# Kernel tuning notes

Hardware: AMD Instinct MI355X
Metric: run time of the kernel (lower is better)

## Reference

```python
import jax, jax.numpy as jnp
import numpy as np

B, L, D_MODEL = 2, 2048, 768
H, F = 12, 16            # num_heads, feature_dim
DH = D_MODEL // H        # head_dim = 64


def setup_inputs() -> dict:
    key = jax.random.key(0)
    ks = jax.random.split(key, 5)
    scale = lambda fan_in: 1.0 / np.sqrt(fan_in)
    return {
        "hidden_states": jax.random.normal(ks[0], (B, L, D_MODEL), jnp.float32),
        "Wq": jax.random.normal(ks[1], (D_MODEL, H * F), jnp.float32) * scale(D_MODEL),
        "Wk": jax.random.normal(ks[2], (D_MODEL, H * F), jnp.float32) * scale(D_MODEL),
        "Wv": jax.random.normal(ks[3], (D_MODEL, H * DH), jnp.float32) * scale(D_MODEL),
        "Wo": jax.random.normal(ks[4], (H * DH, D_MODEL), jnp.float32) * scale(H * DH),
    }


def reference(hidden_states, Wq, Wk, Wv, Wo):
    b, l, d = hidden_states.shape
    dt = hidden_states.dtype
    # projections -> (b, h, l, feat)
    q = (hidden_states @ Wq).reshape(b, l, H, F).transpose(0, 2, 1, 3)
    k = (hidden_states @ Wk).reshape(b, l, H, F).transpose(0, 2, 1, 3)
    v = (hidden_states @ Wv).reshape(b, l, H, DH).transpose(0, 2, 1, 3)

    n = jnp.arange(1, l + 1, dtype=dt)[:, None]          # (l, 1)
    mean_keys = jnp.cumsum(k, axis=2) / n                # running mean over seq
    center_keys = k - mean_keys
    mean_values = jnp.cumsum(v, axis=2) / n
    center_values = v - mean_values

    qK = jnp.einsum('bhqi,bhpi->bhqp', q, center_keys)   # (b,h,l,l)
    causal = jnp.tril(jnp.ones((l, l), dtype=bool))
    qK = jnp.where(causal, qK, jnp.zeros((), dt))

    inv_2d = 1.0 / (2.0 * DH)
    # cumsum over query dim, then sum over key dim (faithful to original)
    qK_squared = jnp.sum(jnp.cumsum(qK * qK * inv_2d, axis=2), axis=3)  # (b,h,l)
    denominator = n[:, 0] + qK_squared                   # (b,h,l) via broadcast

    qKV = jnp.einsum('bhqp,bhpi->bhqi', qK, center_values) / jnp.sqrt(jnp.asarray(DH, dt))
    y = mean_values + qKV / denominator[..., None]       # (b,h,l,dh)
    y = y.transpose(0, 2, 1, 3).reshape(b, l, H * DH)
    return y @ Wo
```

## Files before the change

kernel.cpp:

```cpp
#include <hip/hip_runtime.h>
#include <hip/hip_bf16.h>
#include <stdint.h>

constexpr int B_ = 2, L_ = 2048, DM = 768, NH_ = 12, F_ = 16, DH_ = 64;
constexpr int CH = 32, NCH = L_ / CH;

typedef __bf16 bf16x8 __attribute__((ext_vector_type(8)));
typedef __bf16 bf16x4 __attribute__((ext_vector_type(4)));
typedef float f32x4 __attribute__((ext_vector_type(4)));
typedef float f32x16 __attribute__((ext_vector_type(16)));
typedef unsigned u32x2 __attribute__((ext_vector_type(2)));

#define GLOAD16(g, l)                                                        \
  __builtin_amdgcn_global_load_lds(                                          \
      (const __attribute__((address_space(1))) void*)(g),                    \
      (__attribute__((address_space(3))) void*)(l), 16, 0, 0)

__device__ __forceinline__ unsigned cvt_pk_bf16(float lo, float hi) {
  unsigned r;
  asm("v_cvt_pk_bf16_f32 %0, %1, %2" : "=v"(r) : "v"(lo), "v"(hi));
  return r;
}

union pa_u { unsigned u[4]; bf16x8 v; };

__device__ __forceinline__ void pack_p(const f32x16& s, pa_u& pa0, pa_u& pa1) {
  unsigned w0 = cvt_pk_bf16(s[0], s[1]),   w1 = cvt_pk_bf16(s[2], s[3]);
  unsigned w2 = cvt_pk_bf16(s[4], s[5]),   w3 = cvt_pk_bf16(s[6], s[7]);
  unsigned w4 = cvt_pk_bf16(s[8], s[9]),   w5 = cvt_pk_bf16(s[10], s[11]);
  unsigned w6 = cvt_pk_bf16(s[12], s[13]), w7 = cvt_pk_bf16(s[14], s[15]);
  u32x2 r0 = __builtin_amdgcn_permlane32_swap(w0, w2, false, false);
  u32x2 r1 = __builtin_amdgcn_permlane32_swap(w1, w3, false, false);
  u32x2 r2 = __builtin_amdgcn_permlane32_swap(w4, w6, false, false);
  u32x2 r3 = __builtin_amdgcn_permlane32_swap(w5, w7, false, false);
  pa0.u[0] = r0[0]; pa0.u[1] = r1[0]; pa0.u[2] = r0[1]; pa0.u[3] = r1[1];
  pa1.u[0] = r2[0]; pa1.u[1] = r3[0]; pa1.u[2] = r2[1]; pa1.u[3] = r3[1];
}

__global__ __launch_bounds__(256)
void prep_kernel(const float* __restrict__ hs, const float* __restrict__ Wq,
                 const float* __restrict__ Wk, const float* __restrict__ Wv,
                 const float* __restrict__ Wo, __bf16* __restrict__ hsb,
                 __bf16* __restrict__ WqkvT, __bf16* __restrict__ WoT) {
  int bx = blockIdx.x;
  if (bx < 1440) {
    const float* src; __bf16* dst; int C, kt, nt;
    int id = bx;
    if (id < 144)      { src = Wq; dst = WqkvT;             C = 192; kt = id / 6;  nt = id % 6;  }
    else if (id < 288) { id -= 144; src = Wk; dst = WqkvT + (size_t)192 * 768; C = 192; kt = id / 6;  nt = id % 6;  }
    else if (id < 864) { id -= 288; src = Wv; dst = WqkvT + (size_t)384 * 768; C = 768; kt = id / 24; nt = id % 24; }
    else               { id -= 864; src = Wo; dst = WoT;    C = 768; kt = id / 24; nt = id % 24; }
    __shared__ float ld[32][33];
    int tid = threadIdx.x;
    int r = tid >> 3, cg = tid & 7;
    int k0 = kt * 32, n0 = nt * 32;
    float4 v = *(const float4*)(src + (size_t)(k0 + r) * C + n0 + cg * 4);
    ld[r][cg * 4 + 0] = v.x;
    ld[r][cg * 4 + 1] = v.y;
    ld[r][cg * 4 + 2] = v.z;
    ld[r][cg * 4 + 3] = v.w;
    __syncthreads();
    int nl = tid >> 3, kg = tid & 7;
    bf16x4 o;
#pragma unroll
    for (int j = 0; j < 4; j++) o[j] = (__bf16)ld[kg * 4 + j][nl];
    *(bf16x4*)(dst + (size_t)(n0 + nl) * 768 + k0 + kg * 4) = o;
  } else {
    int base = (bx - 1440) * 2048 + threadIdx.x * 8;
    float4 a = *(const float4*)(hs + base);
    float4 b4 = *(const float4*)(hs + base + 4);
    bf16x8 o;
    o[0] = (__bf16)a.x;  o[1] = (__bf16)a.y;  o[2] = (__bf16)a.z;  o[3] = (__bf16)a.w;
    o[4] = (__bf16)b4.x; o[5] = (__bf16)b4.y; o[6] = (__bf16)b4.z; o[7] = (__bf16)b4.w;
    *(bf16x8*)(hsb + base) = o;
  }
}

template<int BN>
__global__ __launch_bounds__(256)
void gemm_bf16(const __bf16* __restrict__ A, const __bf16* __restrict__ Bt,
               int M, int N, int K, float* __restrict__ C) {
  __shared__ __align__(16) __bf16 Al[2][128 * 32];
  __shared__ __align__(16) __bf16 Bl[2][BN * 32];
  int tid = threadIdx.x;
  int m0 = blockIdx.y * 128, n0 = blockIdx.x * BN;
  int w = tid >> 6, l = tid & 63, lr = l & 15, lg = l >> 4;
  constexpr int MI = (BN == 128) ? 4 : 2;
  int rowb = (BN == 128) ? (w >> 1) * 64 : w * 32;
  int colb = (BN == 128) ? (w & 1) * 64 : 0;
  f32x4 acc[MI][4] = {};
  const __bf16* Ab = A + (size_t)m0 * K;
  const __bf16* Bb = Bt + (size_t)n0 * K;
  int nt = K / 32;

  auto stage = [&](int buf, int k0) {
#pragma unroll
    for (int i = 0; i < 2; i++) {
      int idx = i * 256 + tid;
      GLOAD16(Ab + (size_t)(idx >> 2) * K + k0 + (idx & 3) * 8, &Al[buf][idx * 8]);
    }
    if constexpr (BN == 128) {
#pragma unroll
      for (int i = 0; i < 2; i++) {
        int idx = i * 256 + tid;
        GLOAD16(Bb + (size_t)(idx >> 2) * K + k0 + (idx & 3) * 8, &Bl[buf][idx * 8]);
      }
    } else {
      GLOAD16(Bb + (size_t)(tid >> 2) * K + k0 + (tid & 3) * 8, &Bl[buf][tid * 8]);
    }
  };

  stage(0, 0);
  asm volatile("s_waitcnt vmcnt(0)" ::: "memory");
  __syncthreads();
  int cur = 0;
  for (int t = 0; t < nt; t++) {
    if (t + 1 < nt) stage(cur ^ 1, (t + 1) * 32);
    bf16x8 af[MI], bfr[4];
#pragma unroll
    for (int mi = 0; mi < MI; mi++)
      af[mi] = *(const bf16x8*)&Al[cur][(rowb + mi * 16 + lr) * 32 + lg * 8];
#pragma unroll
    for (int ni = 0; ni < 4; ni++)
      bfr[ni] = *(const bf16x8*)&Bl[cur][(colb + ni * 16 + lr) * 32 + lg * 8];
#pragma unroll
    for (int mi = 0; mi < MI; mi++)
#pragma unroll
      for (int ni = 0; ni < 4; ni++)
        acc[mi][ni] = __builtin_amdgcn_mfma_f32_16x16x32_bf16(
            af[mi], bfr[ni], acc[mi][ni], 0, 0, 0);
    asm volatile("s_waitcnt vmcnt(0)" ::: "memory");
    __syncthreads();
    cur ^= 1;
  }

#pragma unroll
  for (int mi = 0; mi < MI; mi++)
#pragma unroll
    for (int ni = 0; ni < 4; ni++) {
      int n = n0 + colb + ni * 16 + lr;
#pragma unroll
      for (int r = 0; r < 4; r++) {
        int m = m0 + rowb + mi * 16 + lg * 4 + r;
        C[(size_t)m * N + n] = acc[mi][ni][r];
      }
    }
}

__global__ __launch_bounds__(256)
void gemm_proj(const __bf16* __restrict__ A, const __bf16* __restrict__ Bt,
               int K, __bf16* __restrict__ Qh, __bf16* __restrict__ Kh,
               __bf16* __restrict__ Vh, float* __restrict__ csum) {
  __shared__ __align__(16) __bf16 Al[2][128 * 32];
  __shared__ __align__(16) __bf16 Bl[2][64 * 32];
  __shared__ float csl[4][64];
  int tid = threadIdx.x;
  int m0 = blockIdx.y * 128, n0 = blockIdx.x * 64;
  int w = tid >> 6, l = tid & 63, lr = l & 15, lg = l >> 4;
  int rowb = w * 32;
  f32x4 acc[2][4] = {};
  const __bf16* Ab = A + (size_t)m0 * K;
  const __bf16* Bb = Bt + (size_t)n0 * K;
  int nt = K / 32;
  auto stage = [&](int buf, int k0) {
#pragma unroll
    for (int i = 0; i < 2; i++) {
      int idx = i * 256 + tid;
      GLOAD16(Ab + (size_t)(idx >> 2) * K + k0 + (idx & 3) * 8, &Al[buf][idx * 8]);
    }
    GLOAD16(Bb + (size_t)(tid >> 2) * K + k0 + (tid & 3) * 8, &Bl[buf][tid * 8]);
  };
  stage(0, 0);
  asm volatile("s_waitcnt vmcnt(0)" ::: "memory");
  __syncthreads();
  int cur = 0;
  for (int t = 0; t < nt; t++) {
    if (t + 1 < nt) stage(cur ^ 1, (t + 1) * 32);
    bf16x8 af[2], bfr[4];
#pragma unroll
    for (int mi = 0; mi < 2; mi++)
      af[mi] = *(const bf16x8*)&Al[cur][(rowb + mi * 16 + lr) * 32 + lg * 8];
#pragma unroll
    for (int ni = 0; ni < 4; ni++)
      bfr[ni] = *(const bf16x8*)&Bl[cur][(ni * 16 + lr) * 32 + lg * 8];
#pragma unroll
    for (int mi = 0; mi < 2; mi++)
#pragma unroll
      for (int ni = 0; ni < 4; ni++)
        acc[mi][ni] = __builtin_amdgcn_mfma_f32_16x16x32_bf16(
            af[mi], bfr[ni], acc[mi][ni], 0, 0, 0);
    asm volatile("s_waitcnt vmcnt(0)" ::: "memory");
    __syncthreads();
    cur ^= 1;
  }
#pragma unroll
  for (int mi = 0; mi < 2; mi++)
#pragma unroll
    for (int ni = 0; ni < 4; ni++) {
      int n = n0 + ni * 16 + lr;
#pragma unroll
      for (int r = 0; r < 4; r++) {
        int m = m0 + rowb + mi * 16 + lg * 4 + r;
        float v = acc[mi][ni][r];
        int b = m >> 11, ll = m & 2047;
        if (n < 192)
          Qh[((size_t)(b * NH_ + (n >> 4)) * L_ + ll) * F_ + (n & 15)] = (__bf16)v;
        else if (n < 384)
          Kh[((size_t)(b * NH_ + ((n - 192) >> 4)) * L_ + ll) * F_ + ((n - 192) & 15)] = (__bf16)v;
        else
          Vh[((size_t)(b * NH_ + ((n - 384) >> 6)) * L_ + ll) * DH_ + ((n - 384) & 63)] = (__bf16)v;
      }
    }
#pragma unroll
  for (int ni = 0; ni < 4; ni++) {
    float cs = 0.f;
#pragma unroll
    for (int mi = 0; mi < 2; mi++)
#pragma unroll
      for (int r = 0; r < 4; r++) cs += (float)(__bf16)acc[mi][ni][r];
    cs += __shfl_xor(cs, 16, 64);
    cs += __shfl_xor(cs, 32, 64);
    if (lg == 0) csl[w][ni * 16 + lr] = cs;
  }
  __syncthreads();
  {
    int chs = tid >> 6, colg = tid & 63;
    int n = n0 + colg;
    if (n >= 192) {
      int b = m0 >> 11;
      int ch32 = ((m0 & 2047) >> 5) + chs;
      float v = csl[chs][colg];
      int h, c;
      if (n < 384) { h = (n - 192) >> 4; c = (n - 192) & 15; }
      else         { h = (n - 384) >> 6; c = 16 + ((n - 384) & 63); }
      csum[((size_t)(b * NH_ + h) * NCH + ch32) * 80 + c] = v;
    }
  }
}

__global__ __launch_bounds__(128)
void scan_apply(const __bf16* __restrict__ Kh, const __bf16* __restrict__ Vh,
                const float* __restrict__ csum,
                __bf16* __restrict__ CKh, __bf16* __restrict__ CVf,
                __bf16* __restrict__ Yb) {
  int bh = blockIdx.y, ch = blockIdx.x;
  int b = bh / NH_, h = bh % NH_;
  int c = threadIdx.x;
  if (c >= 80) return;
  float run = 0.f;
  for (int j = 0; j < ch; j++) run += csum[((size_t)bh * NCH + j) * 80 + c];
  if (c < 16) {
    const __bf16* src = Kh + ((size_t)bh * L_ + ch * CH) * F_ + c;
    __bf16* ckp = CKh + ((size_t)bh * L_ + ch * CH) * F_ + c;
    for (int r = 0; r < CH; r++) {
      float val = (float)src[(size_t)r * F_];
      run += val;
      float mean = run * __builtin_amdgcn_rcpf((float)(ch * CH + r + 1));
      ckp[(size_t)r * F_] = (__bf16)(val - mean);
    }
  } else {
    int d = c - 16;
    const __bf16* src = Vh + ((size_t)bh * L_ + ch * CH) * DH_ + d;
    __bf16* cvbase = CVf + (size_t)bh * 128 * 1024;
    __bf16* yp = Yb + ((size_t)(b * L_ + ch * CH)) * DM + h * DH_ + d;
    for (int r = 0; r < CH; r++) {
      float val = (float)src[(size_t)r * DH_];
      run += val;
      int p = ch * CH + r;
      float mean = run * __builtin_amdgcn_rcpf((float)(p + 1));
      cvbase[(size_t)(p >> 4) * 1024 + d * 16 + (p & 15)] = (__bf16)(val - mean);
      yp[(size_t)r * DM] = (__bf16)mean;
    }
  }
}

__global__ __launch_bounds__(256)
void attn_mfma(const __bf16* __restrict__ Qh, const __bf16* __restrict__ CKh,
               const __bf16* __restrict__ CVf, __bf16* __restrict__ qkv,
               float* __restrict__ rs2) {
  __shared__ float slab[4][32][65];
  __shared__ float s2slab[4][32];
  int bh = blockIdx.y;
  int pairi = blockIdx.x;
  int tid = threadIdx.x;
  int w = tid >> 6, l = tid & 63;
  int lp = l & 31, hi = l >> 5;
  const __bf16* ckb = CKh + (size_t)bh * L_ * F_;
  const __bf16* cvb = CVf + (size_t)bh * 128 * 1024;

#pragma unroll
  for (int half = 0; half < 2; half++) {
    int ti = half ? (63 - pairi) : pairi;
    int q0 = ti * 32;
    bf16x8 qb = *(const bf16x8*)(Qh + ((size_t)bh * L_ + q0 + lp) * F_ + hi * 8);
    f32x16 pv0 = {}, pv1 = {};
    float s2 = 0.f;

    int pfirst = (w <= ti) ? w : 0;
    bf16x8 ka = *(const bf16x8*)(ckb + (size_t)(pfirst * 32 + lp) * F_ + hi * 8);
    const __bf16* cvp = cvb + (size_t)(2 * pfirst) * 1024 + lp * 16 + hi * 8;
    bf16x8 bv0 = *(const bf16x8*)(cvp);
    bf16x8 bv1 = *(const bf16x8*)(cvp + 512);
    bf16x8 bv2 = *(const bf16x8*)(cvp + 1024);
    bf16x8 bv3 = *(const bf16x8*)(cvp + 1536);

    for (int pt = w; pt <= ti; pt += 4) {
      int ptn = (pt + 4 <= ti) ? pt + 4 : pt;
      bf16x8 ka_n = *(const bf16x8*)(ckb + (size_t)(ptn * 32 + lp) * F_ + hi * 8);
      const __bf16* cvpn = cvb + (size_t)(2 * ptn) * 1024 + lp * 16 + hi * 8;
      bf16x8 bn0 = *(const bf16x8*)(cvpn);
      bf16x8 bn1 = *(const bf16x8*)(cvpn + 512);
      bf16x8 bn2 = *(const bf16x8*)(cvpn + 1024);
      bf16x8 bn3 = *(const bf16x8*)(cvpn + 1536);

      f32x16 s = {};
      s = __builtin_amdgcn_mfma_f32_32x32x16_bf16(ka, qb, s, 0, 0, 0);
      if (pt == ti) {
#pragma unroll
        for (int reg = 0; reg < 16; reg++) {
          int pidx = (reg & 3) + 8 * (reg >> 2) + 4 * hi;
          if (pidx > lp) s[reg] = 0.f;
        }
      }
#pragma unroll
      for (int reg = 0; reg < 16; reg++) s2 = fmaf(s[reg], s[reg], s2);
      pa_u pa0, pa1;
      pack_p(s, pa0, pa1);
      __builtin_amdgcn_s_setprio(1);
      pv0 = __builtin_amdgcn_mfma_f32_32x32x16_bf16(pa0.v, bv0, pv0, 0, 0, 0);
      pv1 = __builtin_amdgcn_mfma_f32_32x32x16_bf16(pa0.v, bv1, pv1, 0, 0, 0);
      pv0 = __builtin_amdgcn_mfma_f32_32x32x16_bf16(pa1.v, bv2, pv0, 0, 0, 0);
      pv1 = __builtin_amdgcn_mfma_f32_32x32x16_bf16(pa1.v, bv3, pv1, 0, 0, 0);
      __builtin_amdgcn_s_setprio(0);
      ka = ka_n; bv0 = bn0; bv1 = bn1; bv2 = bn2; bv3 = bn3;
    }

    s2 += __shfl_xor(s2, 32, 64);
    if (hi == 0) s2slab[w][lp] = s2;
#pragma unroll
    for (int reg = 0; reg < 16; reg++) {
      int ql = (reg & 3) + 8 * (reg >> 2) + 4 * hi;
      slab[w][ql][lp] = pv0[reg];
      slab[w][ql][32 + lp] = pv1[reg];
    }
    __syncthreads();
    if (tid < 32) {
      float v = s2slab[0][tid] + s2slab[1][tid] + s2slab[2][tid] + s2slab[3][tid];
      rs2[(size_t)bh * L_ + q0 + tid] = v * (1.0f / 128.0f);
    }
    {
      int q = tid >> 3, seg = tid & 7;
      bf16x8 o;
#pragma unroll
      for (int j = 0; j < 8; j++) {
        int d = seg * 8 + j;
        float acc = slab[0][q][d] + slab[1][q][d] + slab[2][q][d] + slab[3][q][d];
        o[j] = (__bf16)(acc * 0.125f);
      }
      *(bf16x8*)(qkv + ((size_t)bh * L_ + q0 + q) * DH_ + seg * 8) = o;
    }
    if (half == 0) __syncthreads();
  }
}

__global__ __launch_bounds__(256)
void combine_kernel(const __bf16* __restrict__ qkv, const float* __restrict__ rs2,
                    __bf16* __restrict__ Yb) {
  int bh = blockIdx.y, lt = blockIdx.x;
  int b = bh / NH_, h = bh % NH_;
  int t = threadIdx.x;
  int l0 = lt * 256;
  __shared__ float part[256];
  __shared__ float dinv[256];
  const float* rs = rs2 + (size_t)bh * L_;
  float vals[8];
  float run = 0.f;
#pragma unroll
  for (int i = 0; i < 8; i++) { run += rs[t * 8 + i]; vals[i] = run; }
  part[t] = run;
  __syncthreads();
  for (int o = 1; o < 256; o <<= 1) {
    float add = (t >= o) ? part[t - o] : 0.f;
    __syncthreads();
    part[t] += add;
    __syncthreads();
  }
  float base = (t > 0) ? part[t - 1] : 0.f;
#pragma unroll
  for (int i = 0; i < 8; i++) {
    int ll = t * 8 + i;
    if (ll >= l0 && ll < l0 + 256)
      dinv[ll - l0] = 1.0f / ((float)(ll + 1) + base + vals[i]);
  }
  __syncthreads();
#pragma unroll
  for (int it = 0; it < 8; it++) {
    int v = it * 256 + t;
    int ll = v >> 3, d8 = v & 7;
    bf16x8 q8 = *(const bf16x8*)(qkv + ((size_t)bh * L_ + l0 + ll) * DH_ + d8 * 8);
    __bf16* yp = Yb + ((size_t)(b * L_ + l0 + ll)) * DM + h * DH_ + d8 * 8;
    bf16x8 y8 = *(const bf16x8*)yp;
    float iv = dinv[ll];
#pragma unroll
    for (int j = 0; j < 8; j++)
      y8[j] = (__bf16)((float)y8[j] + (float)q8[j] * iv);
    *(bf16x8*)yp = y8;
  }
}

extern "C" void kernel_launch(void* const* d_in, const int* in_sizes, int n_in,
                              void* d_out, int out_size, void* d_ws, size_t ws_size,
                              hipStream_t stream) {
  const float* hs = (const float*)d_in[0];
  const float* Wq = (const float*)d_in[1];
  const float* Wk = (const float*)d_in[2];
  const float* Wv = (const float*)d_in[3];
  const float* Wo = (const float*)d_in[4];
  float* out = (float*)d_out;
  char* w = (char*)d_ws;

  __bf16* hsb   = (__bf16*)(w);
  __bf16* WqkvT = (__bf16*)(w + 6291456);
  __bf16* WoT   = (__bf16*)(w + 8060928);
  __bf16* Kh    = (__bf16*)(w + 9240576);
  __bf16* Vh    = (__bf16*)(w + 10813440);
  __bf16* qkvb  = (__bf16*)(w + 28114944);
  __bf16* Qh    = (__bf16*)(w + 34406400);
  __bf16* CKh   = (__bf16*)(w + 35979264);
  __bf16* CVfg  = (__bf16*)(w + 37552128);
  __bf16* Yb    = (__bf16*)(w + 43843584);
  float*  rs2   = (float*)(w + 50135040);
  float*  csum  = (float*)(w + 50331648);

  prep_kernel<<<2976, 256, 0, stream>>>(hs, Wq, Wk, Wv, Wo, hsb, WqkvT, WoT);
  dim3 g1(1152 / 64, (B_ * L_) / 128);
  gemm_proj<<<g1, 256, 0, stream>>>(hsb, WqkvT, DM, Qh, Kh, Vh, csum);
  dim3 gs(NCH, B_ * NH_);
  scan_apply<<<gs, 128, 0, stream>>>(Kh, Vh, csum, CKh, CVfg, Yb);
  dim3 g3(32, 24);
  attn_mfma<<<g3, 256, 0, stream>>>(Qh, CKh, CVfg, qkvb, rs2);
  dim3 g5(8, 24);
  combine_kernel<<<g5, 256, 0, stream>>>(qkvb, rs2, Yb);
  dim3 g6(DM / 64, (B_ * L_) / 128);
  gemm_bf16<64><<<g6, 256, 0, stream>>>(Yb, WoT, B_ * L_, DM, DM, out);
}
```

Baseline: 94.95 us.

## Use single-wave 64x64 GEMM tiles without block barriers for both projections

Replaces the 256-thread 128-row GEMM kernels for the QKV projection and output projection with 64-thread single-wavefront kernels, each computing a 64x64 tile with a 4x4 MFMA accumulator grid. With one wave per block, the __syncthreads barriers are dropped and only vmcnt waits order the LDS staging. The grid doubles in blocks, giving more independent waves to fill CUs. Per-wave register use grows and B-tile reuse across waves is lost. The chunk column-sum epilogue now reduces per 32-row pair inside the wave instead of going through shared memory.

```diff
diff --git a/kernel.cpp b/kernel.cpp
--- a/kernel.cpp
+++ b/kernel.cpp
@@ -76,131 +76,62 @@
   }
 }
 
-template<int BN>
-__global__ __launch_bounds__(256)
-void gemm_bf16(const __bf16* __restrict__ A, const __bf16* __restrict__ Bt,
-               int M, int N, int K, float* __restrict__ C) {
-  __shared__ __align__(16) __bf16 Al[2][128 * 32];
-  __shared__ __align__(16) __bf16 Bl[2][BN * 32];
-  int tid = threadIdx.x;
-  int m0 = blockIdx.y * 128, n0 = blockIdx.x * BN;
-  int w = tid >> 6, l = tid & 63, lr = l & 15, lg = l >> 4;
-  constexpr int MI = (BN == 128) ? 4 : 2;
-  int rowb = (BN == 128) ? (w >> 1) * 64 : w * 32;
-  int colb = (BN == 128) ? (w & 1) * 64 : 0;
-  f32x4 acc[MI][4] = {};
-  const __bf16* Ab = A + (size_t)m0 * K;
-  const __bf16* Bb = Bt + (size_t)n0 * K;
-  int nt = K / 32;
+
+__global__ __launch_bounds__(64)
+void gemm_projF(const __bf16* __restrict__ A, const __bf16* __restrict__ Bt,
+                __bf16* __restrict__ Qh, __bf16* __restrict__ Kh,
+                __bf16* __restrict__ Vh, float* __restrict__ csum) {
+  __shared__ __align__(16) __bf16 Al[2][64 * 32];
+  __shared__ __align__(16) __bf16 Bl[2][64 * 32];
+  int l = threadIdx.x, lr = l & 15, lg = l >> 4;
+  int n0 = blockIdx.x * 64, m0 = blockIdx.y * 64;
+  const __bf16* Ab = A + (size_t)m0 * DM;
+  const __bf16* Bb = Bt + (size_t)n0 * DM;
+  f32x4 acc[4][4] = {};
 
   auto stage = [&](int buf, int k0) {
 #pragma unroll
-    for (int i = 0; i < 2; i++) {
-      int idx = i * 256 + tid;
-      GLOAD16(Ab + (size_t)(idx >> 2) * K + k0 + (idx & 3) * 8, &Al[buf][idx * 8]);
-    }
-    if constexpr (BN == 128) {
-#pragma unroll
-      for (int i = 0; i < 2; i++) {
-        int idx = i * 256 + tid;
-        GLOAD16(Bb + (size_t)(idx >> 2) * K + k0 + (idx & 3) * 8, &Bl[buf][idx * 8]);
-      }
-    } else {
-      GLOAD16(Bb + (size_t)(tid >> 2) * K + k0 + (tid & 3) * 8, &Bl[buf][tid * 8]);
+    for (int i = 0; i < 4; i++) {
+      int idx = i * 64 + l;
+      GLOAD16(Ab + (size_t)(idx >> 2) * DM + k0 + (idx & 3) * 8, &Al[buf][idx * 8]);
+    }
+#pragma unroll
+    for (int i = 0; i < 4; i++) {
+      int idx = i * 64 + l;
+      GLOAD16(Bb + (size_t)(idx >> 2) * DM + k0 + (idx & 3) * 8, &Bl[buf][idx * 8]);
     }
   };
 
   stage(0, 0);
   asm volatile("s_waitcnt vmcnt(0)" ::: "memory");
-  __syncthreads();
   int cur = 0;
-  for (int t = 0; t < nt; t++) {
-    if (t + 1 < nt) stage(cur ^ 1, (t + 1) * 32);
-    bf16x8 af[MI], bfr[4];
-#pragma unroll
-    for (int mi = 0; mi < MI; mi++)
-      af[mi] = *(const bf16x8*)&Al[cur][(rowb + mi * 16 + lr) * 32 + lg * 8];
+  for (int t = 0; t < DM / 32; t++) {
+    if (t + 1 < DM / 32) stage(cur ^ 1, (t + 1) * 32);
+    bf16x8 af[4], bf[4];
+#pragma unroll
+    for (int mi = 0; mi < 4; mi++)
+      af[mi] = *(const bf16x8*)&Al[cur][(mi * 16 + lr) * 32 + lg * 8];
 #pragma unroll
     for (int ni = 0; ni < 4; ni++)
-      bfr[ni] = *(const bf16x8*)&Bl[cur][(colb + ni * 16 + lr) * 32 + lg * 8];
-#pragma unroll
-    for (int mi = 0; mi < MI; mi++)
+      bf[ni] = *(const bf16x8*)&Bl[cur][(ni * 16 + lr) * 32 + lg * 8];
+#pragma unroll
+    for (int mi = 0; mi < 4; mi++)
 #pragma unroll
       for (int ni = 0; ni < 4; ni++)
         acc[mi][ni] = __builtin_amdgcn_mfma_f32_16x16x32_bf16(
-            af[mi], bfr[ni], acc[mi][ni], 0, 0, 0);
+            af[mi], bf[ni], acc[mi][ni], 0, 0, 0);
     asm volatile("s_waitcnt vmcnt(0)" ::: "memory");
-    __syncthreads();
     cur ^= 1;
   }
 
 #pragma unroll
-  for (int mi = 0; mi < MI; mi++)
-#pragma unroll
-    for (int ni = 0; ni < 4; ni++) {
-      int n = n0 + colb + ni * 16 + lr;
-#pragma unroll
-      for (int r = 0; r < 4; r++) {
-        int m = m0 + rowb + mi * 16 + lg * 4 + r;
-        C[(size_t)m * N + n] = acc[mi][ni][r];
-      }
-    }
-}
-
-__global__ __launch_bounds__(256)
-void gemm_proj(const __bf16* __restrict__ A, const __bf16* __restrict__ Bt,
-               int K, __bf16* __restrict__ Qh, __bf16* __restrict__ Kh,
-               __bf16* __restrict__ Vh, float* __restrict__ csum) {
-  __shared__ __align__(16) __bf16 Al[2][128 * 32];
-  __shared__ __align__(16) __bf16 Bl[2][64 * 32];
-  __shared__ float csl[4][64];
-  int tid = threadIdx.x;
-  int m0 = blockIdx.y * 128, n0 = blockIdx.x * 64;
-  int w = tid >> 6, l = tid & 63, lr = l & 15, lg = l >> 4;
-  int rowb = w * 32;
-  f32x4 acc[2][4] = {};
-  const __bf16* Ab = A + (size_t)m0 * K;
-  const __bf16* Bb = Bt + (size_t)n0 * K;
-  int nt = K / 32;
-  auto stage = [&](int buf, int k0) {
-#pragma unroll
-    for (int i = 0; i < 2; i++) {
-      int idx = i * 256 + tid;
-      GLOAD16(Ab + (size_t)(idx >> 2) * K + k0 + (idx & 3) * 8, &Al[buf][idx * 8]);
-    }
-    GLOAD16(Bb + (size_t)(tid >> 2) * K + k0 + (tid & 3) * 8, &Bl[buf][tid * 8]);
-  };
-  stage(0, 0);
-  asm volatile("s_waitcnt vmcnt(0)" ::: "memory");
-  __syncthreads();
-  int cur = 0;
-  for (int t = 0; t < nt; t++) {
-    if (t + 1 < nt) stage(cur ^ 1, (t + 1) * 32);
-    bf16x8 af[2], bfr[4];
-#pragma unroll
-    for (int mi = 0; mi < 2; mi++)
-      af[mi] = *(const bf16x8*)&Al[cur][(rowb + mi * 16 + lr) * 32 + lg * 8];
-#pragma unroll
-    for (int ni = 0; ni < 4; ni++)
-      bfr[ni] = *(const bf16x8*)&Bl[cur][(ni * 16 + lr) * 32 + lg * 8];
-#pragma unroll
-    for (int mi = 0; mi < 2; mi++)
-#pragma unroll
-      for (int ni = 0; ni < 4; ni++)
-        acc[mi][ni] = __builtin_amdgcn_mfma_f32_16x16x32_bf16(
-            af[mi], bfr[ni], acc[mi][ni], 0, 0, 0);
-    asm volatile("s_waitcnt vmcnt(0)" ::: "memory");
-    __syncthreads();
-    cur ^= 1;
-  }
-#pragma unroll
-  for (int mi = 0; mi < 2; mi++)
+  for (int mi = 0; mi < 4; mi++)
 #pragma unroll
     for (int ni = 0; ni < 4; ni++) {
       int n = n0 + ni * 16 + lr;
 #pragma unroll
       for (int r = 0; r < 4; r++) {
-        int m = m0 + rowb + mi * 16 + lg * 4 + r;
+        int m = m0 + mi * 16 + lg * 4 + r;
         float v = acc[mi][ni][r];
         int b = m >> 11, ll = m & 2047;
         if (n < 192)
@@ -211,31 +142,89 @@
           Vh[((size_t)(b * NH_ + ((n - 384) >> 6)) * L_ + ll) * DH_ + ((n - 384) & 63)] = (__bf16)v;
       }
     }
+  int b = m0 >> 11;
 #pragma unroll
   for (int ni = 0; ni < 4; ni++) {
-    float cs = 0.f;
-#pragma unroll
-    for (int mi = 0; mi < 2; mi++)
-#pragma unroll
-      for (int r = 0; r < 4; r++) cs += (float)(__bf16)acc[mi][ni][r];
-    cs += __shfl_xor(cs, 16, 64);
-    cs += __shfl_xor(cs, 32, 64);
-    if (lg == 0) csl[w][ni * 16 + lr] = cs;
-  }
-  __syncthreads();
-  {
-    int chs = tid >> 6, colg = tid & 63;
-    int n = n0 + colg;
-    if (n >= 192) {
-      int b = m0 >> 11;
-      int ch32 = ((m0 & 2047) >> 5) + chs;
-      float v = csl[chs][colg];
-      int h, c;
-      if (n < 384) { h = (n - 192) >> 4; c = (n - 192) & 15; }
-      else         { h = (n - 384) >> 6; c = 16 + ((n - 384) & 63); }
-      csum[((size_t)(b * NH_ + h) * NCH + ch32) * 80 + c] = v;
-    }
-  }
+#pragma unroll
+    for (int pair = 0; pair < 2; pair++) {
+      float cs = 0.f;
+#pragma unroll
+      for (int mi = 2 * pair; mi < 2 * pair + 2; mi++)
+#pragma unroll
+        for (int r = 0; r < 4; r++) cs += (float)(__bf16)acc[mi][ni][r];
+      cs += __shfl_xor(cs, 16, 64);
+      cs += __shfl_xor(cs, 32, 64);
+      if (lg == 0) {
+        int n = n0 + ni * 16 + lr;
+        if (n >= 192) {
+          int ch32 = ((m0 & 2047) >> 5) + pair;
+          int h, c;
+          if (n < 384) { h = (n - 192) >> 4; c = (n - 192) & 15; }
+          else         { h = (n - 384) >> 6; c = 16 + ((n - 384) & 63); }
+          csum[((size_t)(b * NH_ + h) * NCH + ch32) * 80 + c] = cs;
+        }
+      }
+    }
+  }
+}
+
+__global__ __launch_bounds__(64)
+void gemm2_sw(const __bf16* __restrict__ A, const __bf16* __restrict__ Bt,
+              float* __restrict__ C) {
+  __shared__ __align__(16) __bf16 Al[2][64 * 32];
+  __shared__ __align__(16) __bf16 Bl[2][64 * 32];
+  int l = threadIdx.x, lr = l & 15, lg = l >> 4;
+  int n0 = blockIdx.x * 64, m0 = blockIdx.y * 64;
+  const __bf16* Ab = A + (size_t)m0 * DM;
+  const __bf16* Bb = Bt + (size_t)n0 * DM;
+  f32x4 acc[4][4] = {};
+
+  auto stage = [&](int buf, int k0) {
+#pragma unroll
+    for (int i = 0; i < 4; i++) {
+      int idx = i * 64 + l;
+      GLOAD16(Ab + (size_t)(idx >> 2) * DM + k0 + (idx & 3) * 8, &Al[buf][idx * 8]);
+    }
+#pragma unroll
+    for (int i = 0; i < 4; i++) {
+      int idx = i * 64 + l;
+      GLOAD16(Bb + (size_t)(idx >> 2) * DM + k0 + (idx & 3) * 8, &Bl[buf][idx * 8]);
+    }
+  };
+
+  stage(0, 0);
+  asm volatile("s_waitcnt vmcnt(0)" ::: "memory");
+  int cur = 0;
+  for (int t = 0; t < DM / 32; t++) {
+    if (t + 1 < DM / 32) stage(cur ^ 1, (t + 1) * 32);
+    bf16x8 af[4], bf[4];
+#pragma unroll
+    for (int mi = 0; mi < 4; mi++)
+      af[mi] = *(const bf16x8*)&Al[cur][(mi * 16 + lr) * 32 + lg * 8];
+#pragma unroll
+    for (int ni = 0; ni < 4; ni++)
+      bf[ni] = *(const bf16x8*)&Bl[cur][(ni * 16 + lr) * 32 + lg * 8];
+#pragma unroll
+    for (int mi = 0; mi < 4; mi++)
+#pragma unroll
+      for (int ni = 0; ni < 4; ni++)
+        acc[mi][ni] = __builtin_amdgcn_mfma_f32_16x16x32_bf16(
+            af[mi], bf[ni], acc[mi][ni], 0, 0, 0);
+    asm volatile("s_waitcnt vmcnt(0)" ::: "memory");
+    cur ^= 1;
+  }
+
+#pragma unroll
+  for (int mi = 0; mi < 4; mi++)
+#pragma unroll
+    for (int ni = 0; ni < 4; ni++) {
+      int n = n0 + ni * 16 + lr;
+#pragma unroll
+      for (int r = 0; r < 4; r++) {
+        int m = m0 + mi * 16 + lg * 4 + r;
+        C[(size_t)m * DM + n] = acc[mi][ni][r];
+      }
+    }
 }
 
 __global__ __launch_bounds__(128)
@@ -433,14 +422,14 @@
   float*  csum  = (float*)(w + 50331648);
 
   prep_kernel<<<2976, 256, 0, stream>>>(hs, Wq, Wk, Wv, Wo, hsb, WqkvT, WoT);
-  dim3 g1(1152 / 64, (B_ * L_) / 128);
-  gemm_proj<<<g1, 256, 0, stream>>>(hsb, WqkvT, DM, Qh, Kh, Vh, csum);
+  dim3 g1(1152 / 64, 4096 / 64);
+  gemm_projF<<<g1, 64, 0, stream>>>(hsb, WqkvT, Qh, Kh, Vh, csum);
   dim3 gs(NCH, B_ * NH_);
   scan_apply<<<gs, 128, 0, stream>>>(Kh, Vh, csum, CKh, CVfg, Yb);
   dim3 g3(32, 24);
   attn_mfma<<<g3, 256, 0, stream>>>(Qh, CKh, CVfg, qkvb, rs2);
   dim3 g5(8, 24);
   combine_kernel<<<g5, 256, 0, stream>>>(qkvb, rs2, Yb);
-  dim3 g6(DM / 64, (B_ * L_) / 128);
-  gemm_bf16<64><<<g6, 256, 0, stream>>>(Yb, WoT, B_ * L_, DM, DM, out);
-}
+  dim3 g6(DM / 64, 4096 / 64);
+  gemm2_sw<<<g6, 64, 0, stream>>>(Yb, WoT, out);
+}
```

Result: slower. 107.0 us (+12.7%).
